# Kernel tuning notes

Hardware: AMD Instinct MI355X
Metric: run time of the kernel (lower is better)

Reference implementation:

```python
import jax, jax.numpy as jnp
import numpy as np

N_NODES = 50000
N_EDGES = 800000
IN_DIM, HID_DIM, OUT_DIM = 128, 64, 64


def spmm(row, col, val, dense):
    # sparse [N,N] (COO) @ dense [N,D] -> [N,D]
    gathered = dense[col] * val[:, None]          # [E, D]
    return jax.ops.segment_sum(gathered, row, num_segments=N_NODES)


def setup_inputs() -> dict:
    key = jax.random.key(0)
    ks = jax.random.split(key, 8)
    stdv1 = 1.0 / np.sqrt(HID_DIM)
    stdv2 = 1.0 / np.sqrt(OUT_DIM)
    return {
        "x": jax.random.normal(ks[0], (N_NODES, IN_DIM), dtype=jnp.float32),
        "edge_row": jax.random.randint(ks[1], (N_EDGES,), 0, N_NODES, dtype=jnp.int32),
        "edge_col": jax.random.randint(ks[2], (N_EDGES,), 0, N_NODES, dtype=jnp.int32),
        "edge_val": jax.random.uniform(ks[3], (N_EDGES,), dtype=jnp.float32),
        "W1": jax.random.uniform(ks[4], (IN_DIM, HID_DIM), jnp.float32, -stdv1, stdv1),
        "b1": jax.random.uniform(ks[5], (HID_DIM,), jnp.float32, -stdv1, stdv1),
        "W2": jax.random.uniform(ks[6], (HID_DIM, OUT_DIM), jnp.float32, -stdv2, stdv2),
        "b2": jax.random.uniform(ks[7], (OUT_DIM,), jnp.float32, -stdv2, stdv2),
    }


def reference(x, edge_row, edge_col, edge_val, W1, b1, W2, b2):
    # layer 1: support = x @ W1; out = adj @ support + b1; relu
    h = jax.nn.relu(spmm(edge_row, edge_col, edge_val, x @ W1) + b1)
    # dropout: eval mode (training=False) -> identity
    # layer 2
    return spmm(edge_row, edge_col, edge_val, h @ W2) + b2
```

## Files before the change

kernel.cpp:

```cpp
#include <hip/hip_runtime.h>


#define N_NODES 50000
#define N_EDGES 800000
#define IN_DIM  128
#define HID_DIM 64
#define OUT_DIM 64

#define RB   256
#define NB   ((N_NODES + RB - 1) / RB)
#define EPB  1024
#define NBLK_E ((N_EDGES + EPB - 1) / EPB)
#define BCAP 5120
#define GEMM_GRID ((N_NODES + 31) / 32)

typedef __attribute__((ext_vector_type(8))) short bf16x8;
typedef __attribute__((ext_vector_type(4))) float f32x4;

__device__ inline unsigned short f2bf(float x) {
    unsigned u = __float_as_uint(x);
    return (unsigned short)((u + 0x7FFFu + ((u >> 16) & 1u)) >> 16);
}
__device__ inline float bf2f(unsigned v) {
    return __uint_as_float(v << 16);
}

__global__ __launch_bounds__(256) void k_prep(
    const float* __restrict__ W1, unsigned short* __restrict__ Wt1,
    const float* __restrict__ W2, unsigned short* __restrict__ Wt2,
    int* __restrict__ bcur)
{
    int b = blockIdx.x, t = threadIdx.x;
    if (b < 32) {
        int e = b * 256 + t;
        int c = e / IN_DIM, k = e % IN_DIM;
        Wt1[c * IN_DIM + k] = f2bf(W1[k * HID_DIM + c]);
    } else if (b < 48) {
        int e2 = (b - 32) * 256 + t;
        int c = e2 / HID_DIM, k = e2 % HID_DIM;
        Wt2[c * HID_DIM + k] = f2bf(W2[k * OUT_DIM + c]);
    } else {
        if (t < NB) bcur[t] = 0;
    }
}

__global__ __launch_bounds__(256) void k_bscatter(
    const int* __restrict__ erow, const int* __restrict__ ecol,
    const float* __restrict__ eval_, int* __restrict__ bcur,
    uint2* __restrict__ bucketed)
{
    __shared__ uint2 sbuf[EPB];
    __shared__ int lc[NB];
    __shared__ int scr[256];
    __shared__ int lbase[NB];
    int t = threadIdx.x;
    if (t < NB) lc[t] = 0;
    __syncthreads();
    int base = blockIdx.x * EPB;
    int ne = min(EPB, N_EDGES - base);
    int bkt[4], rnk[4];
    unsigned w0v[4], vv[4];
    #pragma unroll
    for (int i = 0; i < 4; ++i) {
        int e = base + i * 256 + t;
        bkt[i] = -1;
        if (e < N_EDGES) {
            unsigned r = (unsigned)erow[e];
            bkt[i] = (int)(r >> 8);
            w0v[i] = (unsigned)ecol[e] | ((r & 255u) << 16) | ((r >> 8) << 24);
            vv[i] = __float_as_uint(eval_[e]);
            rnk[i] = atomicAdd(&lc[bkt[i]], 1);
        }
    }
    __syncthreads();
    int cnt = (t < NB) ? lc[t] : 0;
    scr[t] = cnt;
    __syncthreads();
    #pragma unroll
    for (int off = 1; off < 256; off <<= 1) {
        int add = (t >= off) ? scr[t - off] : 0;
        __syncthreads();
        scr[t] += add;
        __syncthreads();
    }
    int excl = scr[t] - cnt;
    __syncthreads();
    scr[t] = excl;
    if (t < NB) lbase[t] = cnt ? atomicAdd(&bcur[t], cnt) : 0;
    __syncthreads();
    #pragma unroll
    for (int i = 0; i < 4; ++i)
        if (bkt[i] >= 0)
            sbuf[scr[bkt[i]] + rnk[i]] = make_uint2(w0v[i], vv[i]);
    __syncthreads();
    #pragma unroll
    for (int i = 0; i < 4; ++i) {
        int idx = i * 256 + t;
        if (idx < ne) {
            uint2 p = sbuf[idx];
            int bk = (int)(p.x >> 24);
            bucketed[(size_t)bk * BCAP + lbase[bk] + (idx - scr[bk])] = p;
        }
    }
}

__global__ __launch_bounds__(256) void k_bfinal(
    const int* __restrict__ bcur, const uint2* __restrict__ bucketed,
    uint2* __restrict__ pairs, int2* __restrict__ offs2)
{
    __shared__ uint2 ebuf[BCAP];
    __shared__ int rcnt[256];
    __shared__ int rsc[256];
    int t = threadIdx.x, b = blockIdx.x;
    int ne = bcur[b];
    int base0 = b * BCAP;
    rcnt[t] = 0;
    __syncthreads();
    for (int i = t; i < ne; i += 256) {
        uint2 p = bucketed[(size_t)base0 + i];
        ebuf[i] = p;
        atomicAdd(&rcnt[(p.x >> 16) & 255], 1);
    }
    __syncthreads();
    int v = rcnt[t];
    rsc[t] = v;
    __syncthreads();
    #pragma unroll
    for (int off = 1; off < 256; off <<= 1) {
        int add = (t >= off) ? rsc[t - off] : 0;
        __syncthreads();
        rsc[t] += add;
        __syncthreads();
    }
    int start = base0 + rsc[t] - v;
    int gr = (b << 8) + t;
    if (gr < N_NODES) offs2[gr] = make_int2(start, start + v);
    rcnt[t] = start;
    __syncthreads();
    for (int i = t; i < ne; i += 256) {
        uint2 p = ebuf[i];
        int pos = atomicAdd(&rcnt[(p.x >> 16) & 255], 1);
        pairs[pos] = make_uint2(p.x & 0xFFFFu, p.y);
    }
}

template <int K, bool IN_BF16>
__device__ __forceinline__ void gemm_body(
    unsigned short* __restrict__ Al, unsigned short* __restrict__ Bl,
    const void* __restrict__ Xv, const unsigned short* __restrict__ Wt,
    unsigned short* __restrict__ out, int bid, int t)
{
    int m0 = bid * 32;
    #pragma unroll
    for (int i = 0; i < K / 32; ++i) {
        int u4 = i * 256 + t;
        int col = (u4 * 8) / K, k = (u4 * 8) % K;
        uint4 w = ((const uint4*)Wt)[u4];
        int byte = (col * K + k) * 2;
        byte ^= ((col & 7) << 4);
        *(uint4*)((char*)Bl + byte) = w;
    }
    if (IN_BF16) {
        const unsigned short* X = (const unsigned short*)Xv;
        int row = t / (K / 8), k = (t % (K / 8)) * 8;
        int grow = m0 + row;
        uint4 v = make_uint4(0, 0, 0, 0);
        if (grow < N_NODES)
            v = *(const uint4*)(X + (size_t)grow * K + k);
        int byte = (row * K + k) * 2;
        byte ^= ((row & 7) << 4);
        *(uint4*)((char*)Al + byte) = v;
    } else {
        const float* X = (const float*)Xv;
        #pragma unroll
        for (int i = 0; i < K / 64; ++i) {
            int f8 = i * 256 + t;
            int row = (f8 * 8) / K, k = (f8 * 8) % K;
            int grow = m0 + row;
            float4 xa = make_float4(0.f, 0.f, 0.f, 0.f), xb = xa;
            if (grow < N_NODES) {
                const float4* src = (const float4*)(X + (size_t)grow * K + k);
                xa = src[0];
                xb = src[1];
            }
            uint4 v;
            v.x = (unsigned)f2bf(xa.x) | ((unsigned)f2bf(xa.y) << 16);
            v.y = (unsigned)f2bf(xa.z) | ((unsigned)f2bf(xa.w) << 16);
            v.z = (unsigned)f2bf(xb.x) | ((unsigned)f2bf(xb.y) << 16);
            v.w = (unsigned)f2bf(xb.z) | ((unsigned)f2bf(xb.w) << 16);
            int byte = (row * K + k) * 2;
            byte ^= ((row & 7) << 4);
            *(uint4*)((char*)Al + byte) = v;
        }
    }
    __syncthreads();

    int w = t >> 6, l = t & 63;
    int lr0 = (w & 1) * 16;
    int c0  = (w >> 1) * 32;
    int lrow = lr0 + (l & 15);
    int kb = (l >> 4) * 8;
    int col0 = c0 + (l & 15), col1 = col0 + 16;
    f32x4 acc0 = {0.f, 0.f, 0.f, 0.f}, acc1 = {0.f, 0.f, 0.f, 0.f};
    #pragma unroll
    for (int kc = 0; kc < K / 32; ++kc) {
        int ka = kc * 32 + kb;
        int ab = (lrow * K + ka) * 2;  ab ^= ((lrow & 7) << 4);
        int bb0 = (col0 * K + ka) * 2; bb0 ^= ((col0 & 7) << 4);
        int bb1 = (col1 * K + ka) * 2; bb1 ^= ((col1 & 7) << 4);
        bf16x8 a  = *(const bf16x8*)((const char*)Al + ab);
        bf16x8 b0 = *(const bf16x8*)((const char*)Bl + bb0);
        bf16x8 b1 = *(const bf16x8*)((const char*)Bl + bb1);
        acc0 = __builtin_amdgcn_mfma_f32_16x16x32_bf16(a, b0, acc0, 0, 0, 0);
        acc1 = __builtin_amdgcn_mfma_f32_16x16x32_bf16(a, b1, acc1, 0, 0, 0);
    }
    int grow0 = m0 + lr0 + (l >> 4) * 4;
    #pragma unroll
    for (int j = 0; j < 4; ++j) {
        int gr = grow0 + j;
        if (gr < N_NODES) {
            out[(size_t)gr * 64 + col0] = f2bf(acc0[j]);
            out[(size_t)gr * 64 + col1] = f2bf(acc1[j]);
        }
    }
}

__global__ __launch_bounds__(256) void k_gemm1(
    const float* __restrict__ X, const unsigned short* __restrict__ Wt,
    unsigned short* __restrict__ out)
{
    __shared__ unsigned short Al[32 * IN_DIM];
    __shared__ unsigned short Bl[64 * IN_DIM];
    gemm_body<IN_DIM, false>(Al, Bl, X, Wt, out, blockIdx.x, threadIdx.x);
}

__global__ __launch_bounds__(256) void k_gemm2(
    const unsigned short* __restrict__ X, const unsigned short* __restrict__ Wt,
    unsigned short* __restrict__ out)
{
    __shared__ unsigned short Al[32 * HID_DIM];
    __shared__ unsigned short Bl[64 * HID_DIM];
    gemm_body<HID_DIM, true>(Al, Bl, X, Wt, out, blockIdx.x, threadIdx.x);
}

template <bool APPLY_RELU, bool OUT_BF16>
__global__ __launch_bounds__(256) void k_gather(
    const int2* __restrict__ offs2, const uint2* __restrict__ pairs,
    const unsigned short* __restrict__ dense, const float* __restrict__ bias,
    void* __restrict__ outp)
{
    int t = threadIdx.x;
    int r = __builtin_amdgcn_readfirstlane(blockIdx.x * 4 + (t >> 6));
    int d = t & 63;
    int2 oe = offs2[r];
    int e0 = oe.x, e1 = oe.y;
    float a[8];
    a[0] = bias[d];
    #pragma unroll
    for (int i = 1; i < 8; ++i) a[i] = 0.f;
    int e = e0;
    for (; e + 8 <= e1; e += 8) {
        uint2 p[8];
        #pragma unroll
        for (int i = 0; i < 8; ++i) p[i] = pairs[e + i];
        unsigned v[8];
        #pragma unroll
        for (int i = 0; i < 8; ++i) v[i] = dense[(size_t)p[i].x * 64u + d];
        #pragma unroll
        for (int i = 0; i < 8; ++i)
            a[i] = fmaf(__uint_as_float(p[i].y), bf2f(v[i]), a[i]);
    }
    if (e + 4 <= e1) {
        uint2 p[4];
        #pragma unroll
        for (int i = 0; i < 4; ++i) p[i] = pairs[e + i];
        unsigned v[4];
        #pragma unroll
        for (int i = 0; i < 4; ++i) v[i] = dense[(size_t)p[i].x * 64u + d];
        #pragma unroll
        for (int i = 0; i < 4; ++i)
            a[i] = fmaf(__uint_as_float(p[i].y), bf2f(v[i]), a[i]);
        e += 4;
    }
    for (; e < e1; ++e) {
        uint2 p = pairs[e];
        a[0] = fmaf(__uint_as_float(p.y),
                    bf2f(dense[(size_t)p.x * 64u + d]), a[0]);
    }
    float acc = ((a[0] + a[1]) + (a[2] + a[3])) +
                ((a[4] + a[5]) + (a[6] + a[7]));
    if (APPLY_RELU) acc = fmaxf(acc, 0.f);
    if (OUT_BF16)
        ((unsigned short*)outp)[(size_t)r * 64 + d] = f2bf(acc);
    else
        ((float*)outp)[(size_t)r * 64 + d] = acc;
}

extern "C" void kernel_launch(void* const* d_in, const int* in_sizes, int n_in,
                              void* d_out, int out_size, void* d_ws, size_t ws_size,
                              hipStream_t stream)
{
    const float* x     = (const float*)d_in[0];
    const int*   erow  = (const int*)d_in[1];
    const int*   ecol  = (const int*)d_in[2];
    const float* eval_ = (const float*)d_in[3];
    const float* W1    = (const float*)d_in[4];
    const float* b1    = (const float*)d_in[5];
    const float* W2    = (const float*)d_in[6];
    const float* b2    = (const float*)d_in[7];
    float* out = (float*)d_out;

    uint2* pairs    = (uint2*)d_ws;
    uint2* bucketed = pairs + (size_t)NB * BCAP;
    unsigned short* support = (unsigned short*)(bucketed + (size_t)NB * BCAP);
    unsigned short* agg1 = support + (size_t)N_NODES * 64;
    unsigned short* Wt1 = agg1 + (size_t)N_NODES * 64;
    unsigned short* Wt2 = Wt1 + IN_DIM * HID_DIM;
    int*  bcur  = (int*)(Wt2 + HID_DIM * OUT_DIM);
    int2* offs2 = (int2*)(bcur + NB);

    const int row_grid = N_NODES / 4;

    k_prep<<<49, 256, 0, stream>>>(W1, Wt1, W2, Wt2, bcur);
    k_bscatter<<<NBLK_E, 256, 0, stream>>>(erow, ecol, eval_, bcur, bucketed);
    k_bfinal<<<NB, 256, 0, stream>>>(bcur, bucketed, pairs, offs2);
    k_gemm1<<<GEMM_GRID, 256, 0, stream>>>(x, Wt1, support);
    k_gather<true, true><<<row_grid, 256, 0, stream>>>(
        offs2, pairs, support, b1, agg1);
    k_gemm2<<<GEMM_GRID, 256, 0, stream>>>(agg1, Wt2, support);
    k_gather<false, false><<<row_grid, 256, 0, stream>>>(
        offs2, pairs, support, b2, out);
}
```

Baseline: 98.86 us.

## Fuse layer-1 gather with layer-2 GEMM in one kernel

Merges the first sparse aggregation (with bias and ReLU) and the second dense GEMM into one kernel. Each 512-thread block gathers 32 rows into shared memory as bf16, then runs MFMA against W2 held in swizzled LDS. This removes a kernel launch and the global write and read of the intermediate activation. In exchange each block processes its 32 rows sequentially per wave (4 rows per wave), which may reduce memory-level parallelism in the gather phase. The output goes to a new workspace buffer.

```diff
diff --git a/kernel.cpp b/kernel.cpp
--- a/kernel.cpp
+++ b/kernel.cpp
@@ -234,20 +234,103 @@
     gemm_body<IN_DIM, false>(Al, Bl, X, Wt, out, blockIdx.x, threadIdx.x);
 }
 
-__global__ __launch_bounds__(256) void k_gemm2(
-    const unsigned short* __restrict__ X, const unsigned short* __restrict__ Wt,
-    unsigned short* __restrict__ out)
-{
-    __shared__ unsigned short Al[32 * HID_DIM];
-    __shared__ unsigned short Bl[64 * HID_DIM];
-    gemm_body<HID_DIM, true>(Al, Bl, X, Wt, out, blockIdx.x, threadIdx.x);
-}
-
-template <bool APPLY_RELU, bool OUT_BF16>
-__global__ __launch_bounds__(256) void k_gather(
+__global__ __launch_bounds__(512) void k_gather_gemm1(
+    const int2* __restrict__ offs2, const uint2* __restrict__ pairs,
+    const unsigned short* __restrict__ dense, const float* __restrict__ b1,
+    const unsigned short* __restrict__ Wt2, unsigned short* __restrict__ out)
+{
+    __shared__ unsigned short Al[32 * 64];
+    __shared__ unsigned short Bl[64 * 64];
+    int t = threadIdx.x;
+    int m0 = blockIdx.x * 32;
+    {
+        int u4 = t;
+        int col = (u4 * 8) / 64, k = (u4 * 8) % 64;
+        uint4 wv = ((const uint4*)Wt2)[u4];
+        int byte = (col * 64 + k) * 2;
+        byte ^= ((col & 7) << 4);
+        *(uint4*)((char*)Bl + byte) = wv;
+    }
+    int w = t >> 6, d = t & 63;
+    #pragma unroll 1
+    for (int j = 0; j < 4; ++j) {
+        int lr = w * 4 + j;
+        int r = __builtin_amdgcn_readfirstlane(m0 + lr);
+        float acc = 0.f;
+        if (r < N_NODES) {
+            int2 oe = offs2[r];
+            int e0 = oe.x, e1 = oe.y;
+            float a[8];
+            a[0] = b1[d];
+            #pragma unroll
+            for (int i = 1; i < 8; ++i) a[i] = 0.f;
+            int e = e0;
+            for (; e + 8 <= e1; e += 8) {
+                uint2 p[8];
+                #pragma unroll
+                for (int i = 0; i < 8; ++i) p[i] = pairs[e + i];
+                unsigned v[8];
+                #pragma unroll
+                for (int i = 0; i < 8; ++i) v[i] = dense[(size_t)p[i].x * 64u + d];
+                #pragma unroll
+                for (int i = 0; i < 8; ++i)
+                    a[i] = fmaf(__uint_as_float(p[i].y), bf2f(v[i]), a[i]);
+            }
+            if (e + 4 <= e1) {
+                uint2 p[4];
+                #pragma unroll
+                for (int i = 0; i < 4; ++i) p[i] = pairs[e + i];
+                unsigned v[4];
+                #pragma unroll
+                for (int i = 0; i < 4; ++i) v[i] = dense[(size_t)p[i].x * 64u + d];
+                #pragma unroll
+                for (int i = 0; i < 4; ++i)
+                    a[i] = fmaf(__uint_as_float(p[i].y), bf2f(v[i]), a[i]);
+                e += 4;
+            }
+            for (; e < e1; ++e) {
+                uint2 p = pairs[e];
+                a[0] = fmaf(__uint_as_float(p.y),
+                            bf2f(dense[(size_t)p.x * 64u + d]), a[0]);
+            }
+            acc = ((a[0] + a[1]) + (a[2] + a[3])) +
+                  ((a[4] + a[5]) + (a[6] + a[7]));
+            acc = fmaxf(acc, 0.f);
+        }
+        int byte = (lr * 64 + d) * 2;
+        byte ^= ((lr & 7) << 4);
+        *(unsigned short*)((char*)Al + byte) = f2bf(acc);
+    }
+    __syncthreads();
+    int l = t & 63;
+    int lr0 = (w & 1) * 16;
+    int c0  = (w >> 1) * 16;
+    int lrow = lr0 + (l & 15);
+    int kb = (l >> 4) * 8;
+    int col = c0 + (l & 15);
+    f32x4 acc0 = {0.f, 0.f, 0.f, 0.f};
+    #pragma unroll
+    for (int kc = 0; kc < 2; ++kc) {
+        int ka = kc * 32 + kb;
+        int ab = (lrow * 64 + ka) * 2; ab ^= ((lrow & 7) << 4);
+        int bb = (col * 64 + ka) * 2;  bb ^= ((col & 7) << 4);
+        bf16x8 a = *(const bf16x8*)((const char*)Al + ab);
+        bf16x8 b = *(const bf16x8*)((const char*)Bl + bb);
+        acc0 = __builtin_amdgcn_mfma_f32_16x16x32_bf16(a, b, acc0, 0, 0, 0);
+    }
+    int grow0 = m0 + lr0 + (l >> 4) * 4;
+    #pragma unroll
+    for (int j = 0; j < 4; ++j) {
+        int gr = grow0 + j;
+        if (gr < N_NODES)
+            out[(size_t)gr * 64 + col] = f2bf(acc0[j]);
+    }
+}
+
+__global__ __launch_bounds__(256) void k_gather2(
     const int2* __restrict__ offs2, const uint2* __restrict__ pairs,
     const unsigned short* __restrict__ dense, const float* __restrict__ bias,
-    void* __restrict__ outp)
+    float* __restrict__ outp)
 {
     int t = threadIdx.x;
     int r = __builtin_amdgcn_readfirstlane(blockIdx.x * 4 + (t >> 6));
@@ -289,11 +372,7 @@
     }
     float acc = ((a[0] + a[1]) + (a[2] + a[3])) +
                 ((a[4] + a[5]) + (a[6] + a[7]));
-    if (APPLY_RELU) acc = fmaxf(acc, 0.f);
-    if (OUT_BF16)
-        ((unsigned short*)outp)[(size_t)r * 64 + d] = f2bf(acc);
-    else
-        ((float*)outp)[(size_t)r * 64 + d] = acc;
+    outp[(size_t)r * 64 + d] = acc;
 }
 
 extern "C" void kernel_launch(void* const* d_in, const int* in_sizes, int n_in,
@@ -313,11 +392,12 @@
     uint2* pairs    = (uint2*)d_ws;
     uint2* bucketed = pairs + (size_t)NB * BCAP;
     unsigned short* support = (unsigned short*)(bucketed + (size_t)NB * BCAP);
-    unsigned short* agg1 = support + (size_t)N_NODES * 64;
-    unsigned short* Wt1 = agg1 + (size_t)N_NODES * 64;
+    unsigned short* Wt1 = support + (size_t)N_NODES * 64;
     unsigned short* Wt2 = Wt1 + IN_DIM * HID_DIM;
     int*  bcur  = (int*)(Wt2 + HID_DIM * OUT_DIM);
     int2* offs2 = (int2*)(bcur + NB);
+
+    unsigned short* support2 = (unsigned short*)(offs2 + N_NODES + 2);
 
     const int row_grid = N_NODES / 4;
 
@@ -325,9 +405,8 @@
     k_bscatter<<<NBLK_E, 256, 0, stream>>>(erow, ecol, eval_, bcur, bucketed);
     k_bfinal<<<NB, 256, 0, stream>>>(bcur, bucketed, pairs, offs2);
     k_gemm1<<<GEMM_GRID, 256, 0, stream>>>(x, Wt1, support);
-    k_gather<true, true><<<row_grid, 256, 0, stream>>>(
-        offs2, pairs, support, b1, agg1);
-    k_gemm2<<<GEMM_GRID, 256, 0, stream>>>(agg1, Wt2, support);
-    k_gather<false, false><<<row_grid, 256, 0, stream>>>(
-        offs2, pairs, support, b2, out);
-}
+    k_gather_gemm1<<<GEMM_GRID, 512, 0, stream>>>(
+        offs2, pairs, support, b1, Wt2, support2);
+    k_gather2<<<row_grid, 256, 0, stream>>>(
+        offs2, pairs, support2, b2, out);
+}
```

Result: faster. 96.68 us (-2.2%).
